# Kernel tuning notes

Hardware: AMD Instinct MI355X
Metric: run time of the kernel (lower is better)

## Reference

```python
import jax, jax.numpy as jnp
import numpy as np

NUM_HEADS = 12


def setup_inputs() -> dict:
    key = jax.random.key(0)
    ks = jax.random.split(key, 6)
    C = 768
    hd = C // NUM_HEADS  # 64
    H = W = 32
    x = jax.random.normal(ks[0], (4, H, W, C), dtype=jnp.float32)
    # Linear weights stored as (in, out) so y = x @ W (+ b)
    Wqkv = jax.random.normal(ks[1], (C, 3 * C), dtype=jnp.float32) * 0.02
    Wproj = jax.random.normal(ks[2], (C, C), dtype=jnp.float32) * 0.02
    bproj = jax.random.normal(ks[3], (C,), dtype=jnp.float32) * 0.02
    rel_pos_h = jax.random.normal(ks[4], (2 * H - 1, hd), dtype=jnp.float32) * 0.02
    rel_pos_w = jax.random.normal(ks[5], (2 * W - 1, hd), dtype=jnp.float32) * 0.02
    return {"x": x, "Wqkv": Wqkv, "Wproj": Wproj, "bproj": bproj,
            "rel_pos_h": rel_pos_h, "rel_pos_w": rel_pos_w}


def _get_rel_pos(size: int, rel_pos: jnp.ndarray) -> jnp.ndarray:
    # q_size == k_size == size; table already has 2*size-1 entries -> no interpolation
    coords = jnp.arange(size)[:, None] - jnp.arange(size)[None, :] + (size - 1)
    return rel_pos[coords]  # (size, size, head_dim)


def reference(x, Wqkv, Wproj, bproj, rel_pos_h, rel_pos_w):
    B, H, W, C = x.shape
    hn = NUM_HEADS
    hd = C // hn
    scale = hd ** (-0.5)
    S = H * W

    qkv = x @ Wqkv                                   # (B,H,W,3C)
    qkv = qkv.reshape(B, S, 3, hn, hd)
    qkv = jnp.transpose(qkv, (2, 0, 3, 1, 4)).reshape(3, B * hn, S, hd)
    q, k, v = qkv[0], qkv[1], qkv[2]                 # each (B*hn, S, hd)

    # decomposed relative position bias
    Rh = _get_rel_pos(H, rel_pos_h)                  # (H,H,hd)
    Rw = _get_rel_pos(W, rel_pos_w)                  # (W,W,hd)
    r_q = q.reshape(B * hn, H, W, hd)
    rel_h = jnp.einsum('bhwc,hkc->bhwk', r_q, Rh)    # (B*hn,H,W,H)
    rel_w = jnp.einsum('bhwc,wkc->bhwk', r_q, Rw)    # (B*hn,H,W,W)
    bias = rel_h[..., :, None] + rel_w[..., None, :] # (B*hn,H,W,H,W)
    bias = bias.reshape(B * hn, S, S)

    scores = scale * jnp.einsum('bqc,bkc->bqk', q, k) + bias
    attn = jax.nn.softmax(scores, axis=-1)
    out = jnp.einsum('bqk,bkc->bqc', attn, v)        # (B*hn,S,hd)

    out = out.reshape(B, hn, H, W, hd)
    out = jnp.transpose(out, (0, 2, 3, 1, 4)).reshape(B, H, W, C)
    return out @ Wproj + bproj
```

## Files before the change

kernel.cpp:

```cpp
#include <hip/hip_runtime.h>
#include <stddef.h>

typedef __bf16 bf16x8 __attribute__((ext_vector_type(8)));
typedef __bf16 bf16x4 __attribute__((ext_vector_type(4)));
typedef float  f32x4  __attribute__((ext_vector_type(4)));

#define MFMA16(a, b, c) __builtin_amdgcn_mfma_f32_16x16x32_bf16((a), (b), (c), 0, 0, 0)

__device__ __forceinline__ void gload_lds16(const void* gsrc, void* ldst) {
    __builtin_amdgcn_global_load_lds(
        (__attribute__((address_space(1))) void*)gsrc,
        (__attribute__((address_space(3))) void*)ldst,
        16, 0, 0);
}

__global__ void cvt_kernel(const float* __restrict__ in, __bf16* __restrict__ out, int n4) {
    int i = blockIdx.x * blockDim.x + threadIdx.x;
    if (i >= n4) return;
    float4 v = ((const float4*)in)[i];
    bf16x4 o = {(__bf16)v.x, (__bf16)v.y, (__bf16)v.z, (__bf16)v.w};
    ((bf16x4*)out)[i] = o;
}

__global__ void transpose_cvt(const float* __restrict__ in, __bf16* __restrict__ out,
                              int R, int C) {
    __shared__ float tile[32][33];
    int c0 = blockIdx.x * 32, r0 = blockIdx.y * 32;
    int tx = threadIdx.x, ty = threadIdx.y;
#pragma unroll
    for (int i = 0; i < 32; i += 8)
        tile[ty + i][tx] = in[(size_t)(r0 + ty + i) * C + c0 + tx];
    __syncthreads();
#pragma unroll
    for (int i = 0; i < 32; i += 8)
        out[(size_t)(c0 + ty + i) * R + r0 + tx] = (__bf16)tile[tx][ty + i];
}

__device__ __forceinline__ void gemm_core_128(
    const __bf16* __restrict__ A, const __bf16* __restrict__ Bt, int K,
    int m0, int n0, __bf16* aT, __bf16* bT, f32x4 acc[4][4]) {
    const int tid  = threadIdx.x;
    const int wid  = tid >> 6, lane = tid & 63;
    const int quad = lane >> 4, l16 = lane & 15;
    const int wm = (wid >> 1) * 64, wn = (wid & 1) * 64;
    const int gchunk = ((tid & 3) ^ ((tid >> 3) & 3)) * 8;
    const __bf16* gA = A  + (size_t)(m0 + (tid >> 2)) * K + gchunk;
    const __bf16* gB = Bt + (size_t)(n0 + (tid >> 2)) * K + gchunk;
    const size_t rows64 = (size_t)64 * K;
    __bf16* lA1 = aT + wid * 512;
    __bf16* lA2 = aT + 2048 + wid * 512;
    __bf16* lB1 = bT + wid * 512;
    __bf16* lB2 = bT + 2048 + wid * 512;
    const int swz = ((quad ^ ((l16 >> 1) & 3)) << 3);
    for (int k0 = 0; k0 < K; k0 += 32) {
        __syncthreads();
        gload_lds16(gA + k0, lA1);
        gload_lds16(gA + rows64 + k0, lA2);
        gload_lds16(gB + k0, lB1);
        gload_lds16(gB + rows64 + k0, lB2);
        __syncthreads();
        bf16x8 af[4], bfr[4];
#pragma unroll
        for (int t = 0; t < 4; t++) {
            af[t]  = *(const bf16x8*)(aT + (wm + t * 16 + l16) * 32 + swz);
            bfr[t] = *(const bf16x8*)(bT + (wn + t * 16 + l16) * 32 + swz);
        }
#pragma unroll
        for (int rt = 0; rt < 4; rt++)
#pragma unroll
            for (int ct = 0; ct < 4; ct++)
                acc[rt][ct] = MFMA16(af[rt], bfr[ct], acc[rt][ct]);
    }
}

__global__ __launch_bounds__(256, 2)
void gemm_qkv_kernel(const __bf16* __restrict__ A, const __bf16* __restrict__ Bt,
                     __bf16* __restrict__ qb, __bf16* __restrict__ kb,
                     __bf16* __restrict__ vtb) {
    __shared__ __bf16 aT[4096], bT[4096];
    f32x4 acc[4][4];
#pragma unroll
    for (int i = 0; i < 4; i++)
#pragma unroll
        for (int j = 0; j < 4; j++) { f32x4 z = {0.f, 0.f, 0.f, 0.f}; acc[i][j] = z; }
    const int m0 = blockIdx.x * 128, n0 = blockIdx.y * 128;
    gemm_core_128(A, Bt, 768, m0, n0, aT, bT, acc);
    const int tid = threadIdx.x, wid = tid >> 6, lane = tid & 63;
    const int quad = lane >> 4, l16 = lane & 15;
    const int wm = (wid >> 1) * 64, wn = (wid & 1) * 64;
#pragma unroll
    for (int rt = 0; rt < 4; rt++)
#pragma unroll
        for (int ct = 0; ct < 4; ct++) {
            const int ng = n0 + wn + ct * 16 + l16;
            const int which = ng / 768;
            const int rem = ng - which * 768;
            const int hh = rem >> 6, d = rem & 63;
#pragma unroll
            for (int r = 0; r < 4; r++) {
                const int mg = m0 + wm + rt * 16 + quad * 4 + r;
                const int b = mg >> 10, s = mg & 1023;
                const int bh = b * 12 + hh;
                __bf16 bv = (__bf16)acc[rt][ct][r];
                if (which == 0)      qb[((size_t)bh * 1024 + s) * 64 + d] = bv;
                else if (which == 1) kb[((size_t)bh * 1024 + s) * 64 + d] = bv;
                else                 vtb[((size_t)bh * 64 + d) * 1024 + s] = bv;
            }
        }
}

__global__ __launch_bounds__(256, 2)
void gemm_proj_kernel(const __bf16* __restrict__ A, const __bf16* __restrict__ Bt,
                      const float* __restrict__ bias, float* __restrict__ out) {
    __shared__ __bf16 aT[4096], bT[4096];
    f32x4 acc[4][4];
#pragma unroll
    for (int i = 0; i < 4; i++)
#pragma unroll
        for (int j = 0; j < 4; j++) { f32x4 z = {0.f, 0.f, 0.f, 0.f}; acc[i][j] = z; }
    const int m0 = blockIdx.x * 128, n0 = blockIdx.y * 128;
    gemm_core_128(A, Bt, 768, m0, n0, aT, bT, acc);
    const int tid = threadIdx.x, wid = tid >> 6, lane = tid & 63;
    const int quad = lane >> 4, l16 = lane & 15;
    const int wm = (wid >> 1) * 64, wn = (wid & 1) * 64;
#pragma unroll
    for (int rt = 0; rt < 4; rt++)
#pragma unroll
        for (int ct = 0; ct < 4; ct++) {
            const int ng = n0 + wn + ct * 16 + l16;
            const float bb = bias[ng];
#pragma unroll
            for (int r = 0; r < 4; r++) {
                const int mg = m0 + wm + rt * 16 + quad * 4 + r;
                out[(size_t)mg * 768 + ng] = acc[rt][ct][r] + bb;
            }
        }
}

__global__ __launch_bounds__(256, 2)
void relpos_kernel(const __bf16* __restrict__ q, const float* __restrict__ rph,
                   const float* __restrict__ rpw, float* __restrict__ rel_h,
                   float* __restrict__ rel_w) {
    const int tid = threadIdx.x, wid = tid >> 6, lane = tid & 63;
    const int quad = lane >> 4, l16 = lane & 15;
    const int bx = blockIdx.x;
    const int isW = blockIdx.y;
    const int bh = bx >> 5, fix = bx & 31;
    const int mi = (wid >> 1) * 16, ni = (wid & 1) * 16;
    const int m = mi + l16;
    const int s_a = isW ? (m * 32 + fix) : (fix * 32 + m);
    const __bf16* qp = q + ((size_t)bh * 1024 + s_a) * 64;
    bf16x8 a0 = *(const bf16x8*)(qp + quad * 8);
    bf16x8 a1 = *(const bf16x8*)(qp + 32 + quad * 8);
    const int n = ni + l16;
    const float* tb = (isW ? rpw : rph) + (size_t)(fix - n + 31) * 64;
    float4 t0 = *(const float4*)(tb + quad * 8);
    float4 t1 = *(const float4*)(tb + quad * 8 + 4);
    float4 t2 = *(const float4*)(tb + 32 + quad * 8);
    float4 t3 = *(const float4*)(tb + 32 + quad * 8 + 4);
    bf16x8 b0 = {(__bf16)t0.x, (__bf16)t0.y, (__bf16)t0.z, (__bf16)t0.w,
                 (__bf16)t1.x, (__bf16)t1.y, (__bf16)t1.z, (__bf16)t1.w};
    bf16x8 b1 = {(__bf16)t2.x, (__bf16)t2.y, (__bf16)t2.z, (__bf16)t2.w,
                 (__bf16)t3.x, (__bf16)t3.y, (__bf16)t3.z, (__bf16)t3.w};
    f32x4 acc = {0.f, 0.f, 0.f, 0.f};
    acc = MFMA16(a0, b0, acc);
    acc = MFMA16(a1, b1, acc);
    float* op = isW ? rel_w : rel_h;
#pragma unroll
    for (int r = 0; r < 4; r++) {
        int mo = mi + quad * 4 + r;
        int so = isW ? (mo * 32 + fix) : (fix * 32 + mo);
        op[((size_t)bh * 1024 + so) * 32 + n] = acc[r];
    }
}

__global__ __launch_bounds__(256, 2)
void attn_kernel(const __bf16* __restrict__ q, const __bf16* __restrict__ kk,
                 const __bf16* __restrict__ vt, const float* __restrict__ rel_h,
                 const float* __restrict__ rel_w, __bf16* __restrict__ aout) {
    __shared__ __bf16 kbuf[4096];
    __shared__ __bf16 vbuf[4096];
    __shared__ __bf16 pbuf[4][16 * 72];
    __shared__ float  relh[64][32];
    const int tid = threadIdx.x, wid = tid >> 6, lane = tid & 63;
    const int quad = lane >> 4, l16 = lane & 15;
    const int qt = blockIdx.x, bh = blockIdx.y;
    const int b = bh / 12, hh = bh - b * 12;
    const int q0 = qt * 64;
    const int r_base = wid * 16 + quad * 4;

    {
        int rr = tid >> 2, cc = (tid & 3) * 8;
        const float* sh = rel_h + ((size_t)bh * 1024 + q0 + rr) * 32 + cc;
        *(float4*)(&relh[rr][cc])     = *(const float4*)sh;
        *(float4*)(&relh[rr][cc + 4]) = *(const float4*)(sh + 4);
    }

    float bw0[4], bw1[4];
#pragma unroll
    for (int r = 0; r < 4; r++) {
        const float* pw = rel_w + ((size_t)bh * 1024 + q0 + r_base + r) * 32;
        bw0[r] = pw[l16];
        bw1[r] = pw[16 + l16];
    }

    const __bf16* qp = q + ((size_t)bh * 1024 + q0 + wid * 16 + l16) * 64;
    bf16x8 aq0 = *(const bf16x8*)(qp + quad * 8);
    bf16x8 aq1 = *(const bf16x8*)(qp + 32 + quad * 8);

    float l_run[4];
    f32x4 o_acc[4];
#pragma unroll
    for (int r = 0; r < 4; r++) l_run[r] = 0.f;
#pragma unroll
    for (int t = 0; t < 4; t++) { f32x4 z = {0.f, 0.f, 0.f, 0.f}; o_acc[t] = z; }

    const __bf16* kg0 = kk + (size_t)bh * 65536;
    const __bf16* vg0 = vt + (size_t)bh * 65536;
    const int c1 = wid, c2 = wid + 4;
    const int srow = lane >> 3;
    const int scol = (((lane & 7) ^ srow)) * 8;
    const int swz0 = ((quad ^ (l16 & 7)) << 3);
    const int swz1 = (((quad | 4) ^ (l16 & 7)) << 3);
    __bf16* pw = pbuf[wid];

    __syncthreads();

    for (int kt = 0; kt < 16; kt++) {
        __syncthreads();
        const __bf16* kg = kg0 + kt * 64 * 64;
        const __bf16* vg = vg0 + kt * 64;
        gload_lds16(kg + (c1 * 8 + srow) * 64 + scol, kbuf + c1 * 512);
        gload_lds16(kg + (c2 * 8 + srow) * 64 + scol, kbuf + c2 * 512);
        gload_lds16(vg + (size_t)(c1 * 8 + srow) * 1024 + scol, vbuf + c1 * 512);
        gload_lds16(vg + (size_t)(c2 * 8 + srow) * 1024 + scol, vbuf + c2 * 512);
        __syncthreads();

        f32x4 sacc[4];
#pragma unroll
        for (int ct = 0; ct < 4; ct++) {
            const int key = ct * 16 + l16;
            bf16x8 bk0 = *(const bf16x8*)(kbuf + key * 64 + swz0);
            bf16x8 bk1 = *(const bf16x8*)(kbuf + key * 64 + swz1);
            f32x4 z = {0.f, 0.f, 0.f, 0.f};
            z = MFMA16(aq0, bk0, z);
            z = MFMA16(aq1, bk1, z);
            sacc[ct] = z;
        }

        float bh0[4], bh1[4];
#pragma unroll
        for (int r = 0; r < 4; r++) {
            bh0[r] = relh[r_base + r][kt * 2];
            bh1[r] = relh[r_base + r][kt * 2 + 1];
        }

#pragma unroll
        for (int ct = 0; ct < 4; ct++)
#pragma unroll
            for (int r = 0; r < 4; r++) {
                float sv = fmaf(sacc[ct][r], 0.125f,
                                (ct < 2 ? bh0[r] : bh1[r]) + ((ct & 1) ? bw1[r] : bw0[r]));
                float p = __expf(sv);
                l_run[r] += p;
                pw[(quad * 4 + r) * 72 + ct * 16 + l16] = (__bf16)p;
            }

        bf16x8 ap0 = *(const bf16x8*)(pw + l16 * 72 + quad * 8);
        bf16x8 ap1 = *(const bf16x8*)(pw + l16 * 72 + 32 + quad * 8);
#pragma unroll
        for (int nt = 0; nt < 4; nt++) {
            const int d = nt * 16 + l16;
            bf16x8 bv0 = *(const bf16x8*)(vbuf + d * 64 + swz0);
            bf16x8 bv1 = *(const bf16x8*)(vbuf + d * 64 + swz1);
            o_acc[nt] = MFMA16(ap0, bv0, o_acc[nt]);
            o_acc[nt] = MFMA16(ap1, bv1, o_acc[nt]);
        }
    }

#pragma unroll
    for (int r = 0; r < 4; r++) {
        float s = l_run[r];
        s += __shfl_xor(s, 1);
        s += __shfl_xor(s, 2);
        s += __shfl_xor(s, 4);
        s += __shfl_xor(s, 8);
        l_run[r] = 1.f / s;
    }
    const int srow_o = q0 + wid * 16 + quad * 4;
#pragma unroll
    for (int nt = 0; nt < 4; nt++)
#pragma unroll
        for (int r = 0; r < 4; r++) {
            float v = o_acc[nt][r] * l_run[r];
            aout[((size_t)b * 1024 + srow_o + r) * 768 + hh * 64 + nt * 16 + l16] = (__bf16)v;
        }
}

extern "C" void kernel_launch(void* const* d_in, const int* in_sizes, int n_in,
                              void* d_out, int out_size, void* d_ws, size_t ws_size,
                              hipStream_t stream) {
    const float* x     = (const float*)d_in[0];
    const float* Wqkv  = (const float*)d_in[1];
    const float* Wproj = (const float*)d_in[2];
    const float* bproj = (const float*)d_in[3];
    const float* rph   = (const float*)d_in[4];
    const float* rpw   = (const float*)d_in[5];
    float* out = (float*)d_out;
    char* ws = (char*)d_ws;

    __bf16* xbf    = (__bf16*)(ws);
    __bf16* WqkvT  = (__bf16*)(ws + 6291456);
    __bf16* WprojT = (__bf16*)(ws + 9830400);
    __bf16* qb     = (__bf16*)(ws + 11010048);
    __bf16* kb     = (__bf16*)(ws + 17301504);
    __bf16* vtb    = (__bf16*)(ws + 23592960);
    float*  rel_h  = (float*)(ws + 29884416);
    float*  rel_w  = (float*)(ws + 36175872);
    __bf16* aob    = (__bf16*)(ws + 42467328);

    cvt_kernel<<<dim3(3072), dim3(256), 0, stream>>>(x, xbf, 786432);
    transpose_cvt<<<dim3(72, 24), dim3(32, 8), 0, stream>>>(Wqkv, WqkvT, 768, 2304);
    transpose_cvt<<<dim3(24, 24), dim3(32, 8), 0, stream>>>(Wproj, WprojT, 768, 768);
    gemm_qkv_kernel<<<dim3(32, 18), dim3(256), 0, stream>>>(xbf, WqkvT, qb, kb, vtb);
    relpos_kernel<<<dim3(1536, 2), dim3(256), 0, stream>>>(qb, rph, rpw, rel_h, rel_w);
    attn_kernel<<<dim3(16, 48), dim3(256), 0, stream>>>(qb, kb, vtb, rel_h, rel_w, aob);
    gemm_proj_kernel<<<dim3(32, 6), dim3(256), 0, stream>>>(aob, WprojT, bproj, out);
}
```

Measured before the change: 170.0 us.

## Fuse prep kernels, widen GEMM K-tile to 64, double attention query tile

Three conversion/transpose launches are merged into one prep kernel to cut launch overhead. The GEMM core now stages a 64-wide K slice per sync with a new XOR swizzle, halving barrier count. The attention kernel processes 128 queries per block (two 16-row tiles per wave), reusing each K/V tile load across twice as many queries and halving grid size. Launch bounds move to 3 blocks/SM, which may increase register pressure, and the larger tiles mean fewer blocks to fill the GPU.

```diff
diff --git a/kernel.cpp b/kernel.cpp
--- a/kernel.cpp
+++ b/kernel.cpp
@@ -14,19 +14,24 @@
         16, 0, 0);
 }
 
-__global__ void cvt_kernel(const float* __restrict__ in, __bf16* __restrict__ out, int n4) {
-    int i = blockIdx.x * blockDim.x + threadIdx.x;
-    if (i >= n4) return;
-    float4 v = ((const float4*)in)[i];
-    bf16x4 o = {(__bf16)v.x, (__bf16)v.y, (__bf16)v.z, (__bf16)v.w};
-    ((bf16x4*)out)[i] = o;
-}
-
-__global__ void transpose_cvt(const float* __restrict__ in, __bf16* __restrict__ out,
-                              int R, int C) {
+__global__ void prep_kernel(const float* __restrict__ x, __bf16* __restrict__ xbf,
+                            const float* __restrict__ Wqkv, __bf16* __restrict__ WqkvT,
+                            const float* __restrict__ Wproj, __bf16* __restrict__ WprojT) {
     __shared__ float tile[32][33];
-    int c0 = blockIdx.x * 32, r0 = blockIdx.y * 32;
-    int tx = threadIdx.x, ty = threadIdx.y;
+    const int bx = blockIdx.x, tid = threadIdx.x;
+    if (bx < 3072) {
+        int i = bx * 256 + tid;
+        float4 v = ((const float4*)x)[i];
+        bf16x4 o = {(__bf16)v.x, (__bf16)v.y, (__bf16)v.z, (__bf16)v.w};
+        ((bf16x4*)xbf)[i] = o;
+        return;
+    }
+    const float* in; __bf16* out; int R, C, c0, r0;
+    if (bx < 4800) { int bb = bx - 3072; in = Wqkv;  out = WqkvT;  R = 768; C = 2304;
+                     c0 = (bb % 72) * 32; r0 = (bb / 72) * 32; }
+    else           { int bb = bx - 4800; in = Wproj; out = WprojT; R = 768; C = 768;
+                     c0 = (bb % 24) * 32; r0 = (bb / 24) * 32; }
+    const int tx = tid & 31, ty = tid >> 5;
 #pragma unroll
     for (int i = 0; i < 32; i += 8)
         tile[ty + i][tx] = in[(size_t)(r0 + ty + i) * C + c0 + tx];
@@ -36,55 +41,56 @@
         out[(size_t)(c0 + ty + i) * R + r0 + tx] = (__bf16)tile[tx][ty + i];
 }
 
-__device__ __forceinline__ void gemm_core_128(
+__device__ __forceinline__ void gemm_core_bk64(
     const __bf16* __restrict__ A, const __bf16* __restrict__ Bt, int K,
     int m0, int n0, __bf16* aT, __bf16* bT, f32x4 acc[4][4]) {
     const int tid  = threadIdx.x;
     const int wid  = tid >> 6, lane = tid & 63;
     const int quad = lane >> 4, l16 = lane & 15;
     const int wm = (wid >> 1) * 64, wn = (wid & 1) * 64;
-    const int gchunk = ((tid & 3) ^ ((tid >> 3) & 3)) * 8;
-    const __bf16* gA = A  + (size_t)(m0 + (tid >> 2)) * K + gchunk;
-    const __bf16* gB = Bt + (size_t)(n0 + (tid >> 2)) * K + gchunk;
-    const size_t rows64 = (size_t)64 * K;
-    __bf16* lA1 = aT + wid * 512;
-    __bf16* lA2 = aT + 2048 + wid * 512;
-    __bf16* lB1 = bT + wid * 512;
-    __bf16* lB2 = bT + 2048 + wid * 512;
-    const int swz = ((quad ^ ((l16 >> 1) & 3)) << 3);
-    for (int k0 = 0; k0 < K; k0 += 32) {
+    const int r_in = lane >> 3;
+    const int cswz = ((lane & 7) ^ r_in) * 8;
+    const __bf16* gA = A  + (size_t)(m0 + wid * 8 + r_in) * K + cswz;
+    const __bf16* gB = Bt + (size_t)(n0 + wid * 8 + r_in) * K + cswz;
+    const int sA = (l16 & 7);
+    for (int k0 = 0; k0 < K; k0 += 64) {
         __syncthreads();
-        gload_lds16(gA + k0, lA1);
-        gload_lds16(gA + rows64 + k0, lA2);
-        gload_lds16(gB + k0, lB1);
-        gload_lds16(gB + rows64 + k0, lB2);
+#pragma unroll
+        for (int j = 0; j < 4; j++) {
+            gload_lds16(gA + (size_t)(j * 32) * K + k0, aT + (j * 32 + wid * 8) * 64);
+            gload_lds16(gB + (size_t)(j * 32) * K + k0, bT + (j * 32 + wid * 8) * 64);
+        }
         __syncthreads();
-        bf16x8 af[4], bfr[4];
-#pragma unroll
-        for (int t = 0; t < 4; t++) {
-            af[t]  = *(const bf16x8*)(aT + (wm + t * 16 + l16) * 32 + swz);
-            bfr[t] = *(const bf16x8*)(bT + (wn + t * 16 + l16) * 32 + swz);
-        }
-#pragma unroll
-        for (int rt = 0; rt < 4; rt++)
-#pragma unroll
-            for (int ct = 0; ct < 4; ct++)
-                acc[rt][ct] = MFMA16(af[rt], bfr[ct], acc[rt][ct]);
-    }
-}
-
-__global__ __launch_bounds__(256, 2)
+#pragma unroll
+        for (int kh = 0; kh < 2; kh++) {
+            bf16x8 af[4], bfr[4];
+#pragma unroll
+            for (int t = 0; t < 4; t++) {
+                const int slot = ((kh * 4 + quad) ^ sA) << 3;
+                af[t]  = *(const bf16x8*)(aT + (wm + t * 16 + l16) * 64 + slot);
+                bfr[t] = *(const bf16x8*)(bT + (wn + t * 16 + l16) * 64 + slot);
+            }
+#pragma unroll
+            for (int rt = 0; rt < 4; rt++)
+#pragma unroll
+                for (int ct = 0; ct < 4; ct++)
+                    acc[rt][ct] = MFMA16(af[rt], bfr[ct], acc[rt][ct]);
+        }
+    }
+}
+
+__global__ __launch_bounds__(256, 3)
 void gemm_qkv_kernel(const __bf16* __restrict__ A, const __bf16* __restrict__ Bt,
                      __bf16* __restrict__ qb, __bf16* __restrict__ kb,
                      __bf16* __restrict__ vtb) {
-    __shared__ __bf16 aT[4096], bT[4096];
+    __shared__ __bf16 aT[8192], bT[8192];
     f32x4 acc[4][4];
 #pragma unroll
     for (int i = 0; i < 4; i++)
 #pragma unroll
         for (int j = 0; j < 4; j++) { f32x4 z = {0.f, 0.f, 0.f, 0.f}; acc[i][j] = z; }
     const int m0 = blockIdx.x * 128, n0 = blockIdx.y * 128;
-    gemm_core_128(A, Bt, 768, m0, n0, aT, bT, acc);
+    gemm_core_bk64(A, Bt, 768, m0, n0, aT, bT, acc);
     const int tid = threadIdx.x, wid = tid >> 6, lane = tid & 63;
     const int quad = lane >> 4, l16 = lane & 15;
     const int wm = (wid >> 1) * 64, wn = (wid & 1) * 64;
@@ -109,17 +115,17 @@
         }
 }
 
-__global__ __launch_bounds__(256, 2)
+__global__ __launch_bounds__(256, 3)
 void gemm_proj_kernel(const __bf16* __restrict__ A, const __bf16* __restrict__ Bt,
                       const float* __restrict__ bias, float* __restrict__ out) {
-    __shared__ __bf16 aT[4096], bT[4096];
+    __shared__ __bf16 aT[8192], bT[8192];
     f32x4 acc[4][4];
 #pragma unroll
     for (int i = 0; i < 4; i++)
 #pragma unroll
         for (int j = 0; j < 4; j++) { f32x4 z = {0.f, 0.f, 0.f, 0.f}; acc[i][j] = z; }
     const int m0 = blockIdx.x * 128, n0 = blockIdx.y * 128;
-    gemm_core_128(A, Bt, 768, m0, n0, aT, bT, acc);
+    gemm_core_bk64(A, Bt, 768, m0, n0, aT, bT, acc);
     const int tid = threadIdx.x, wid = tid >> 6, lane = tid & 63;
     const int quad = lane >> 4, l16 = lane & 15;
     const int wm = (wid >> 1) * 64, wn = (wid & 1) * 64;
@@ -174,52 +180,64 @@
     }
 }
 
-__global__ __launch_bounds__(256, 2)
+__global__ __launch_bounds__(256, 3)
 void attn_kernel(const __bf16* __restrict__ q, const __bf16* __restrict__ kk,
                  const __bf16* __restrict__ vt, const float* __restrict__ rel_h,
                  const float* __restrict__ rel_w, __bf16* __restrict__ aout) {
     __shared__ __bf16 kbuf[4096];
     __shared__ __bf16 vbuf[4096];
-    __shared__ __bf16 pbuf[4][16 * 72];
-    __shared__ float  relh[64][32];
+    __shared__ __bf16 pbuf[4][32 * 72];
+    __shared__ float  relh[128][32];
     const int tid = threadIdx.x, wid = tid >> 6, lane = tid & 63;
     const int quad = lane >> 4, l16 = lane & 15;
     const int qt = blockIdx.x, bh = blockIdx.y;
     const int b = bh / 12, hh = bh - b * 12;
-    const int q0 = qt * 64;
-    const int r_base = wid * 16 + quad * 4;
+    const int q0 = qt * 128;
+    const int w0 = wid * 32;
 
     {
-        int rr = tid >> 2, cc = (tid & 3) * 8;
+        int rr = tid >> 1, cc = (tid & 1) * 16;
         const float* sh = rel_h + ((size_t)bh * 1024 + q0 + rr) * 32 + cc;
-        *(float4*)(&relh[rr][cc])     = *(const float4*)sh;
-        *(float4*)(&relh[rr][cc + 4]) = *(const float4*)(sh + 4);
-    }
-
-    float bw0[4], bw1[4];
-#pragma unroll
-    for (int r = 0; r < 4; r++) {
-        const float* pw = rel_w + ((size_t)bh * 1024 + q0 + r_base + r) * 32;
-        bw0[r] = pw[l16];
-        bw1[r] = pw[16 + l16];
-    }
-
-    const __bf16* qp = q + ((size_t)bh * 1024 + q0 + wid * 16 + l16) * 64;
-    bf16x8 aq0 = *(const bf16x8*)(qp + quad * 8);
-    bf16x8 aq1 = *(const bf16x8*)(qp + 32 + quad * 8);
-
-    float l_run[4];
-    f32x4 o_acc[4];
-#pragma unroll
-    for (int r = 0; r < 4; r++) l_run[r] = 0.f;
-#pragma unroll
-    for (int t = 0; t < 4; t++) { f32x4 z = {0.f, 0.f, 0.f, 0.f}; o_acc[t] = z; }
+        *(float4*)(&relh[rr][cc])      = *(const float4*)sh;
+        *(float4*)(&relh[rr][cc + 4])  = *(const float4*)(sh + 4);
+        *(float4*)(&relh[rr][cc + 8])  = *(const float4*)(sh + 8);
+        *(float4*)(&relh[rr][cc + 12]) = *(const float4*)(sh + 12);
+    }
+
+    float bw[2][2][4];
+#pragma unroll
+    for (int rt = 0; rt < 2; rt++)
+#pragma unroll
+        for (int r = 0; r < 4; r++) {
+            const float* pw = rel_w + ((size_t)bh * 1024 + q0 + w0 + rt * 16 + quad * 4 + r) * 32;
+            bw[rt][0][r] = pw[l16];
+            bw[rt][1][r] = pw[16 + l16];
+        }
+
+    bf16x8 aq[2][2];
+#pragma unroll
+    for (int rt = 0; rt < 2; rt++) {
+        const __bf16* qp = q + ((size_t)bh * 1024 + q0 + w0 + rt * 16 + l16) * 64;
+        aq[rt][0] = *(const bf16x8*)(qp + quad * 8);
+        aq[rt][1] = *(const bf16x8*)(qp + 32 + quad * 8);
+    }
+
+    float l_run[2][4];
+    f32x4 o_acc[2][4];
+#pragma unroll
+    for (int rt = 0; rt < 2; rt++)
+#pragma unroll
+        for (int r = 0; r < 4; r++) l_run[rt][r] = 0.f;
+#pragma unroll
+    for (int rt = 0; rt < 2; rt++)
+#pragma unroll
+        for (int t = 0; t < 4; t++) { f32x4 z = {0.f, 0.f, 0.f, 0.f}; o_acc[rt][t] = z; }
 
     const __bf16* kg0 = kk + (size_t)bh * 65536;
     const __bf16* vg0 = vt + (size_t)bh * 65536;
     const int c1 = wid, c2 = wid + 4;
     const int srow = lane >> 3;
-    const int scol = (((lane & 7) ^ srow)) * 8;
+    const int scol = ((lane & 7) ^ srow) * 8;
     const int swz0 = ((quad ^ (l16 & 7)) << 3);
     const int swz1 = (((quad | 4) ^ (l16 & 7)) << 3);
     __bf16* pw = pbuf[wid];
@@ -236,65 +254,80 @@
         gload_lds16(vg + (size_t)(c2 * 8 + srow) * 1024 + scol, vbuf + c2 * 512);
         __syncthreads();
 
-        f32x4 sacc[4];
+        bf16x8 bk[4][2];
 #pragma unroll
         for (int ct = 0; ct < 4; ct++) {
             const int key = ct * 16 + l16;
-            bf16x8 bk0 = *(const bf16x8*)(kbuf + key * 64 + swz0);
-            bf16x8 bk1 = *(const bf16x8*)(kbuf + key * 64 + swz1);
-            f32x4 z = {0.f, 0.f, 0.f, 0.f};
-            z = MFMA16(aq0, bk0, z);
-            z = MFMA16(aq1, bk1, z);
-            sacc[ct] = z;
-        }
-
-        float bh0[4], bh1[4];
-#pragma unroll
-        for (int r = 0; r < 4; r++) {
-            bh0[r] = relh[r_base + r][kt * 2];
-            bh1[r] = relh[r_base + r][kt * 2 + 1];
-        }
-
-#pragma unroll
-        for (int ct = 0; ct < 4; ct++)
+            bk[ct][0] = *(const bf16x8*)(kbuf + key * 64 + swz0);
+            bk[ct][1] = *(const bf16x8*)(kbuf + key * 64 + swz1);
+        }
+
+#pragma unroll
+        for (int rt = 0; rt < 2; rt++) {
+            f32x4 sacc[4];
+#pragma unroll
+            for (int ct = 0; ct < 4; ct++) {
+                f32x4 z = {0.f, 0.f, 0.f, 0.f};
+                z = MFMA16(aq[rt][0], bk[ct][0], z);
+                z = MFMA16(aq[rt][1], bk[ct][1], z);
+                sacc[ct] = z;
+            }
+            float bh0[4], bh1[4];
 #pragma unroll
             for (int r = 0; r < 4; r++) {
-                float sv = fmaf(sacc[ct][r], 0.125f,
-                                (ct < 2 ? bh0[r] : bh1[r]) + ((ct & 1) ? bw1[r] : bw0[r]));
-                float p = __expf(sv);
-                l_run[r] += p;
-                pw[(quad * 4 + r) * 72 + ct * 16 + l16] = (__bf16)p;
-            }
-
-        bf16x8 ap0 = *(const bf16x8*)(pw + l16 * 72 + quad * 8);
-        bf16x8 ap1 = *(const bf16x8*)(pw + l16 * 72 + 32 + quad * 8);
+                bh0[r] = relh[w0 + rt * 16 + quad * 4 + r][kt * 2];
+                bh1[r] = relh[w0 + rt * 16 + quad * 4 + r][kt * 2 + 1];
+            }
+#pragma unroll
+            for (int ct = 0; ct < 4; ct++)
+#pragma unroll
+                for (int r = 0; r < 4; r++) {
+                    float sv = fmaf(sacc[ct][r], 0.125f,
+                                    (ct < 2 ? bh0[r] : bh1[r]) +
+                                    ((ct & 1) ? bw[rt][1][r] : bw[rt][0][r]));
+                    float p = __expf(sv);
+                    l_run[rt][r] += p;
+                    pw[(rt * 16 + quad * 4 + r) * 72 + ct * 16 + l16] = (__bf16)p;
+                }
+        }
+
 #pragma unroll
         for (int nt = 0; nt < 4; nt++) {
             const int d = nt * 16 + l16;
             bf16x8 bv0 = *(const bf16x8*)(vbuf + d * 64 + swz0);
             bf16x8 bv1 = *(const bf16x8*)(vbuf + d * 64 + swz1);
-            o_acc[nt] = MFMA16(ap0, bv0, o_acc[nt]);
-            o_acc[nt] = MFMA16(ap1, bv1, o_acc[nt]);
-        }
-    }
-
-#pragma unroll
-    for (int r = 0; r < 4; r++) {
-        float s = l_run[r];
-        s += __shfl_xor(s, 1);
-        s += __shfl_xor(s, 2);
-        s += __shfl_xor(s, 4);
-        s += __shfl_xor(s, 8);
-        l_run[r] = 1.f / s;
-    }
-    const int srow_o = q0 + wid * 16 + quad * 4;
-#pragma unroll
-    for (int nt = 0; nt < 4; nt++)
+#pragma unroll
+            for (int rt = 0; rt < 2; rt++) {
+                bf16x8 ap0 = *(const bf16x8*)(pw + (rt * 16 + l16) * 72 + quad * 8);
+                bf16x8 ap1 = *(const bf16x8*)(pw + (rt * 16 + l16) * 72 + 32 + quad * 8);
+                o_acc[rt][nt] = MFMA16(ap0, bv0, o_acc[rt][nt]);
+                o_acc[rt][nt] = MFMA16(ap1, bv1, o_acc[rt][nt]);
+            }
+        }
+    }
+
+#pragma unroll
+    for (int rt = 0; rt < 2; rt++)
 #pragma unroll
         for (int r = 0; r < 4; r++) {
-            float v = o_acc[nt][r] * l_run[r];
-            aout[((size_t)b * 1024 + srow_o + r) * 768 + hh * 64 + nt * 16 + l16] = (__bf16)v;
-        }
+            float s = l_run[rt][r];
+            s += __shfl_xor(s, 1);
+            s += __shfl_xor(s, 2);
+            s += __shfl_xor(s, 4);
+            s += __shfl_xor(s, 8);
+            l_run[rt][r] = 1.f / s;
+        }
+#pragma unroll
+    for (int rt = 0; rt < 2; rt++) {
+        const int srow_o = q0 + w0 + rt * 16 + quad * 4;
+#pragma unroll
+        for (int nt = 0; nt < 4; nt++)
+#pragma unroll
+            for (int r = 0; r < 4; r++) {
+                float v = o_acc[rt][nt][r] * l_run[rt][r];
+                aout[((size_t)b * 1024 + srow_o + r) * 768 + hh * 64 + nt * 16 + l16] = (__bf16)v;
+            }
+    }
 }
 
 extern "C" void kernel_launch(void* const* d_in, const int* in_sizes, int n_in,
@@ -319,11 +352,9 @@
     float*  rel_w  = (float*)(ws + 36175872);
     __bf16* aob    = (__bf16*)(ws + 42467328);
 
-    cvt_kernel<<<dim3(3072), dim3(256), 0, stream>>>(x, xbf, 786432);
-    transpose_cvt<<<dim3(72, 24), dim3(32, 8), 0, stream>>>(Wqkv, WqkvT, 768, 2304);
-    transpose_cvt<<<dim3(24, 24), dim3(32, 8), 0, stream>>>(Wproj, WprojT, 768, 768);
+    prep_kernel<<<dim3(5376), dim3(256), 0, stream>>>(x, xbf, Wqkv, WqkvT, Wproj, WprojT);
     gemm_qkv_kernel<<<dim3(32, 18), dim3(256), 0, stream>>>(xbf, WqkvT, qb, kb, vtb);
     relpos_kernel<<<dim3(1536, 2), dim3(256), 0, stream>>>(qb, rph, rpw, rel_h, rel_w);
-    attn_kernel<<<dim3(16, 48), dim3(256), 0, stream>>>(qb, kb, vtb, rel_h, rel_w, aob);
+    attn_kernel<<<dim3(8, 48), dim3(256), 0, stream>>>(qb, kb, vtb, rel_h, rel_w, aob);
     gemm_proj_kernel<<<dim3(32, 6), dim3(256), 0, stream>>>(aob, WprojT, bproj, out);
 }
```

Measured after the change: 165.8 us. -2.4%, faster.
